# Kernel optimization log

Measured on AMD Instinct MI355X. Metric: run time of the kernel, lower is better.

Reference implementation:

```python
import jax, jax.numpy as jnp
import numpy as np

HEAD_NUM = 8
KEY_DIM = 16
EMBEDDING_DIM = 128
LOGIT_CLIPPING = 10.0

B, G, P, E = 512, 100, 100, 128


def setup_inputs() -> dict:
    key = jax.random.key(0)
    ks = jax.random.split(key, 9)
    return {
        "input1": jax.random.normal(ks[0], (B, 1, E), jnp.float32),
        "input2": jax.random.normal(ks[1], (B, G, E), jnp.float32),
        "remaining_loaded": jax.random.uniform(ks[2], (B, G, 1), jnp.float32),
        "ninf_mask": jnp.zeros((B, G, P), jnp.float32),
        "encoded_nodes": jax.random.normal(ks[3], (B, P, E), jnp.float32),
        "Wq": jax.random.normal(ks[4], (2 * E + 1, HEAD_NUM * KEY_DIM), jnp.float32) * 0.05,
        "Wk": jax.random.normal(ks[5], (E, HEAD_NUM * KEY_DIM), jnp.float32) * 0.05,
        "Wv": jax.random.normal(ks[6], (E, HEAD_NUM * KEY_DIM), jnp.float32) * 0.05,
        "Wc": jax.random.normal(ks[7], (HEAD_NUM * KEY_DIM, E), jnp.float32) * 0.05,
        "bc": jnp.zeros((E,), jnp.float32),
    }


def _heads(x):  # [B, N, H*K] -> [B, H, N, K]
    b, n, _ = x.shape
    return x.reshape(b, n, HEAD_NUM, KEY_DIM).transpose(0, 2, 1, 3)


def reference(input1, input2, remaining_loaded, ninf_mask, encoded_nodes, Wq, Wk, Wv, Wc, bc):
    group_s = input2.shape[1]
    # reset(): precompute keys/values from encoded nodes
    k = _heads(encoded_nodes @ Wk)  # [B,H,P,K]
    v = _heads(encoded_nodes @ Wv)  # [B,H,P,K]
    # forward()
    input_cat = jnp.concatenate(
        [jnp.broadcast_to(input1, (input1.shape[0], group_s, input1.shape[2])),
         input2, remaining_loaded], axis=2)  # [B,G,2E+1]
    q = _heads(input_cat @ Wq)  # [B,H,G,K]
    # multi-head attention with additive ninf mask
    score = jnp.einsum("bhgk,bhpk->bhgp", q, k) / np.sqrt(KEY_DIM).astype(np.float32)
    score = score + ninf_mask[:, None, :, :]
    weights = jax.nn.softmax(score, axis=3)
    out = jnp.einsum("bhgp,bhpk->bhgk", weights, v)  # [B,H,G,K]
    out_concat = out.transpose(0, 2, 1, 3).reshape(out.shape[0], group_s, HEAD_NUM * KEY_DIM)
    mh_atten_out = out_concat @ Wc + bc  # [B,G,E]
    # single-head pointer scoring with tanh clipping
    score2 = jnp.einsum("bge,bpe->bgp", mh_atten_out, encoded_nodes) / np.sqrt(EMBEDDING_DIM).astype(np.float32)
    score_masked = LOGIT_CLIPPING * jnp.tanh(score2) + ninf_mask
    probs = jax.nn.softmax(score_masked, axis=2)
    return probs
```

## Files before the change

kernel.cpp:

```cpp
#include <hip/hip_runtime.h>

#define NB 512
#define NG 100
#define NP 100
#define NE 128
#define NH 8

typedef __attribute__((ext_vector_type(8))) short short8;
typedef __attribute__((ext_vector_type(4))) short short4v;
typedef __attribute__((ext_vector_type(4))) float f32x4;

#define SE_STRIDE 128
#define SK_STRIDE 128
#define SVT_STRIDE 112
#define SE_BASE 0
#define SK_BASE (100 * 128)
#define SVT_BASE (SK_BASE + 100 * 128)
#define SMEM_SHORTS (SVT_BASE + 128 * 112)
#define SMEM_BYTES (SMEM_SHORTS * 2)

__device__ __forceinline__ short f2bf(float f) {
    union { float f; unsigned u; } v; v.f = f;
    unsigned r = v.u + 0x7FFFu + ((v.u >> 16) & 1u);
    return (short)(r >> 16);
}

__device__ __forceinline__ f32x4 mfma16(short4v a, short4v b, f32x4 c) {
#if __has_builtin(__builtin_amdgcn_mfma_f32_16x16x16_bf16)
    return __builtin_amdgcn_mfma_f32_16x16x16_bf16(a, b, c, 0, 0, 0);
#elif __has_builtin(__builtin_amdgcn_mfma_f32_16x16x16bf16_1k)
    return __builtin_amdgcn_mfma_f32_16x16x16bf16_1k(a, b, c, 0, 0, 0);
#else
    f32x4 d;
    asm volatile("v_mfma_f32_16x16x16_bf16 %0, %1, %2, %3"
                 : "=&v"(d) : "v"(a), "v"(b), "v"(c));
    return d;
#endif
}

__device__ __forceinline__ f32x4 mfma32(short8 a, short8 b, f32x4 c) {
    return __builtin_amdgcn_mfma_f32_16x16x32_bf16(a, b, c, 0, 0, 0);
}

__global__ void prep_kernel(const float* __restrict__ Wq, const float* __restrict__ Wk,
                            const float* __restrict__ Wv, const float* __restrict__ Wc,
                            short* __restrict__ WqT2, short* __restrict__ WkT,
                            short* __restrict__ WvT, short* __restrict__ WcT,
                            short* __restrict__ WqT1)
{
    int idx = blockIdx.x * 256 + threadIdx.x;
    int mat = idx >> 14;
    int e   = idx & 16383;
    int k = e >> 7, n = e & 127;
    float v;
    short* dst;
    if (mat == 0)      { v = Wq[(128 + k) * 128 + n]; dst = WqT2; }
    else if (mat == 1) { v = Wk[k * 128 + n];         dst = WkT;  }
    else if (mat == 2) { v = Wv[k * 128 + n];         dst = WvT;  }
    else if (mat == 3) { v = Wc[k * 128 + n];         dst = WcT;  }
    else               { v = Wq[k * 128 + n];         dst = WqT1; }
    dst[n * 128 + k] = f2bf(v);
}

__global__ __launch_bounds__(448, 2)
void fused_kernel(const float* __restrict__ input1, const float* __restrict__ input2,
                  const float* __restrict__ rem, const float* __restrict__ mask,
                  const float* __restrict__ enc, const float* __restrict__ Wq,
                  const float* __restrict__ bc,
                  const short* __restrict__ WqT2, const short* __restrict__ WkT,
                  const short* __restrict__ WvT, const short* __restrict__ WcT,
                  const short* __restrict__ WqT1, float* __restrict__ out)
{
    extern __shared__ short smem[];

    const int b    = blockIdx.x;
    const int tid  = threadIdx.x;
    const int wave = tid >> 6, lane = tid & 63;
    const int l16  = lane & 15, lh = lane >> 4;
    const int gt   = wave;
    const int g    = gt * 16 + l16;
    const bool gok = (g < NG);
    const float NINF = -__builtin_inff();

    {
        const f32x4* e4 = (const f32x4*)(enc + (size_t)b * NP * NE);
        for (int idx = tid; idx < NP * 32; idx += 448) {
            int row = idx >> 5, c = idx & 31;
            f32x4 v = e4[idx];
            short4v h = { f2bf(v[0]), f2bf(v[1]), f2bf(v[2]), f2bf(v[3]) };
            int off = (row * SE_STRIDE + c * 4) ^ ((row & 15) << 2);
            *(short4v*)(smem + SE_BASE + off) = h;
        }
        for (int idx = tid; idx < 128 * 3; idx += 448) {
            int row = idx / 3, c = 100 + (idx % 3) * 4;
            int off = (row * SVT_STRIDE + c) ^ ((row & 15) << 2);
            *(short4v*)(smem + SVT_BASE + off) = (short4v){0, 0, 0, 0};
        }
    }

    short4v qb[8];
    {
        const float* xrow = input2 + ((size_t)b * NG + g) * NE;
        const float* i1   = input1 + (size_t)b * NE;
        short8 xb[4], yb[4];
        #pragma unroll
        for (int ks = 0; ks < 4; ++ks) {
            f32x4 v0 = {0.f,0.f,0.f,0.f}, v1 = {0.f,0.f,0.f,0.f};
            if (gok) {
                v0 = *(const f32x4*)(xrow + ks * 32 + lh * 8);
                v1 = *(const f32x4*)(xrow + ks * 32 + lh * 8 + 4);
            }
            xb[ks] = (short8){ f2bf(v0[0]), f2bf(v0[1]), f2bf(v0[2]), f2bf(v0[3]),
                               f2bf(v1[0]), f2bf(v1[1]), f2bf(v1[2]), f2bf(v1[3]) };
            f32x4 u0 = *(const f32x4*)(i1 + ks * 32 + lh * 8);
            f32x4 u1 = *(const f32x4*)(i1 + ks * 32 + lh * 8 + 4);
            yb[ks] = (short8){ f2bf(u0[0]), f2bf(u0[1]), f2bf(u0[2]), f2bf(u0[3]),
                               f2bf(u1[0]), f2bf(u1[1]), f2bf(u1[2]), f2bf(u1[3]) };
        }
        float remv = gok ? rem[(size_t)b * NG + g] : 0.f;
        #pragma unroll
        for (int nt = 0; nt < 8; ++nt) {
            f32x4 acc0 = {0.f, 0.f, 0.f, 0.f}, acc1 = {0.f, 0.f, 0.f, 0.f};
            #pragma unroll
            for (int ks = 0; ks < 4; ++ks) {
                short8 a2 = *(const short8*)(WqT2 + (nt * 16 + l16) * NE + ks * 32 + lh * 8);
                acc0 = mfma32(a2, xb[ks], acc0);
                short8 a1 = *(const short8*)(WqT1 + (nt * 16 + l16) * NE + ks * 32 + lh * 8);
                acc1 = mfma32(a1, yb[ks], acc1);
            }
            f32x4 wlv = *(const f32x4*)(Wq + 256 * NE + nt * 16 + lh * 4);
            short4v q;
            #pragma unroll
            for (int r = 0; r < 4; ++r)
                q[r] = f2bf(0.25f * (acc0[r] + acc1[r] + remv * wlv[r]));
            qb[nt] = q;
        }
    }
    __syncthreads();

    for (int t = wave; t < 112; t += 7) {
        int mat = (t >= 56);
        int tt  = mat ? t - 56 : t;
        int mt = tt >> 3, nt = tt & 7;
        const short* WT = mat ? WvT : WkT;
        int arow = mt * 16 + l16;
        bool aok = (arow < NP);
        f32x4 acc0 = {0.f, 0.f, 0.f, 0.f}, acc1 = {0.f, 0.f, 0.f, 0.f};
        #pragma unroll
        for (int kt = 0; kt < 8; ++kt) {
            short4v a = {0, 0, 0, 0};
            if (aok) {
                int off = (arow * SE_STRIDE + kt * 16 + lh * 4) ^ ((arow & 15) << 2);
                a = *(const short4v*)(smem + SE_BASE + off);
            }
            short4v w = *(const short4v*)(WT + (nt * 16 + l16) * NE + kt * 16 + lh * 4);
            if (kt < 4) acc0 = mfma16(a, w, acc0);
            else        acc1 = mfma16(a, w, acc1);
        }
        f32x4 acc = acc0 + acc1;
        if (!mat) {
            #pragma unroll
            for (int r = 0; r < 4; ++r) {
                int p = mt * 16 + lh * 4 + r;
                if (p < NP) {
                    int off = (p * SK_STRIDE + nt * 16 + l16) ^ ((p & 15) << 2);
                    smem[SK_BASE + off] = f2bf(acc[r]);
                }
            }
        } else {
            int vrow = nt * 16 + l16;
            int p0 = mt * 16 + lh * 4;
            if (p0 < NP) {
                short4v h = { f2bf(acc[0]), f2bf(acc[1]), f2bf(acc[2]), f2bf(acc[3]) };
                int off = (vrow * SVT_STRIDE + p0) ^ ((vrow & 15) << 2);
                *(short4v*)(smem + SVT_BASE + off) = h;
            }
        }
    }

    float mk[7][4];
    {
        const float* mrow = mask + ((size_t)b * NG + g) * NP;
        #pragma unroll
        for (int pt = 0; pt < 7; ++pt)
            #pragma unroll
            for (int r = 0; r < 4; ++r) {
                int p = pt * 16 + lh * 4 + r;
                mk[pt][r] = (gok && p < NP) ? mrow[p] : NINF;
            }
    }
    __syncthreads();

    short4v ocb[8];
    #pragma unroll
    for (int h = 0; h < NH; ++h) {
        float vals[7][4];
        #pragma unroll
        for (int pt = 0; pt < 7; ++pt) {
            int prow = pt * 16 + l16;
            int off = (prow * SK_STRIDE + h * 16 + lh * 4) ^ ((prow & 15) << 2);
            short4v kf = *(const short4v*)(smem + SK_BASE + off);
            f32x4 z = {0.f, 0.f, 0.f, 0.f};
            f32x4 sc = mfma16(kf, qb[h], z);
            bool pv = (pt < 6) || (lh == 0);
            #pragma unroll
            for (int r = 0; r < 4; ++r)
                vals[pt][r] = pv ? sc[r] + mk[pt][r] : NINF;
        }
        float mr0 = vals[0][0], mr1 = vals[0][1], mr2 = vals[0][2], mr3 = vals[0][3];
        #pragma unroll
        for (int pt = 1; pt < 7; ++pt) {
            mr0 = fmaxf(mr0, vals[pt][0]); mr1 = fmaxf(mr1, vals[pt][1]);
            mr2 = fmaxf(mr2, vals[pt][2]); mr3 = fmaxf(mr3, vals[pt][3]);
        }
        float m = fmaxf(fmaxf(mr0, mr1), fmaxf(mr2, mr3));
        m = fmaxf(m, __shfl_xor(m, 16));
        m = fmaxf(m, __shfl_xor(m, 32));
        float s0 = 0.f, s1 = 0.f, s2 = 0.f, s3 = 0.f;
        #pragma unroll
        for (int pt = 0; pt < 7; ++pt) {
            float e0 = __expf(vals[pt][0] - m); vals[pt][0] = e0; s0 += e0;
            float e1 = __expf(vals[pt][1] - m); vals[pt][1] = e1; s1 += e1;
            float e2 = __expf(vals[pt][2] - m); vals[pt][2] = e2; s2 += e2;
            float e3 = __expf(vals[pt][3] - m); vals[pt][3] = e3; s3 += e3;
        }
        float s = (s0 + s1) + (s2 + s3);
        s += __shfl_xor(s, 16);
        s += __shfl_xor(s, 32);
        float inv = 1.f / s;
        f32x4 o0 = {0.f, 0.f, 0.f, 0.f}, o1 = {0.f, 0.f, 0.f, 0.f};
        #pragma unroll
        for (int pt = 0; pt < 7; ++pt) {
            short4v pb = { f2bf(vals[pt][0] * inv), f2bf(vals[pt][1] * inv),
                           f2bf(vals[pt][2] * inv), f2bf(vals[pt][3] * inv) };
            int vrow = h * 16 + l16;
            int off = (vrow * SVT_STRIDE + pt * 16 + lh * 4) ^ ((vrow & 15) << 2);
            short4v vf = *(const short4v*)(smem + SVT_BASE + off);
            if (pt & 1) o1 = mfma16(vf, pb, o1);
            else        o0 = mfma16(vf, pb, o0);
        }
        f32x4 o = o0 + o1;
        ocb[h] = (short4v){ f2bf(o[0]), f2bf(o[1]), f2bf(o[2]), f2bf(o[3]) };
    }

    short4v mhb[8];
    #pragma unroll
    for (int nt = 0; nt < 8; ++nt) {
        f32x4 acc0 = {0.f, 0.f, 0.f, 0.f}, acc1 = {0.f, 0.f, 0.f, 0.f};
        #pragma unroll
        for (int kt = 0; kt < 8; ++kt) {
            short4v a = *(const short4v*)(WcT + (nt * 16 + l16) * NE + kt * 16 + lh * 4);
            if (kt < 4) acc0 = mfma16(a, ocb[kt], acc0);
            else        acc1 = mfma16(a, ocb[kt], acc1);
        }
        f32x4 acc = acc0 + acc1;
        f32x4 bcv = *(const f32x4*)(bc + nt * 16 + lh * 4);
        mhb[nt] = (short4v){ f2bf((acc[0] + bcv[0]) * 0.08838834764831845f),
                             f2bf((acc[1] + bcv[1]) * 0.08838834764831845f),
                             f2bf((acc[2] + bcv[2]) * 0.08838834764831845f),
                             f2bf((acc[3] + bcv[3]) * 0.08838834764831845f) };
    }

    const float* mrow = mask + ((size_t)b * NG + g) * NP;
    float vals2[7][4];
    #pragma unroll
    for (int pt = 0; pt < 7; ++pt) {
        int prow = pt * 16 + l16;
        f32x4 acc0 = {0.f, 0.f, 0.f, 0.f}, acc1 = {0.f, 0.f, 0.f, 0.f};
        #pragma unroll
        for (int kt = 0; kt < 8; ++kt) {
            int off = (prow * SE_STRIDE + kt * 16 + lh * 4) ^ ((prow & 15) << 2);
            short4v ef = *(const short4v*)(smem + SE_BASE + off);
            if (kt < 4) acc0 = mfma16(ef, mhb[kt], acc0);
            else        acc1 = mfma16(ef, mhb[kt], acc1);
        }
        f32x4 acc = acc0 + acc1;
        #pragma unroll
        for (int r = 0; r < 4; ++r) {
            int p = pt * 16 + lh * 4 + r;
            bool pv = gok && (p < NP);
            float mkv = pv ? mrow[p] : NINF;
            float x = acc[r];
            float th = 1.f - 2.f / (__expf(2.f * x) + 1.f);
            vals2[pt][r] = pv ? 10.f * th + mkv : NINF;
        }
    }
    {
        float mr0 = vals2[0][0], mr1 = vals2[0][1], mr2 = vals2[0][2], mr3 = vals2[0][3];
        #pragma unroll
        for (int pt = 1; pt < 7; ++pt) {
            mr0 = fmaxf(mr0, vals2[pt][0]); mr1 = fmaxf(mr1, vals2[pt][1]);
            mr2 = fmaxf(mr2, vals2[pt][2]); mr3 = fmaxf(mr3, vals2[pt][3]);
        }
        float m = fmaxf(fmaxf(mr0, mr1), fmaxf(mr2, mr3));
        m = fmaxf(m, __shfl_xor(m, 16));
        m = fmaxf(m, __shfl_xor(m, 32));
        float s0 = 0.f, s1 = 0.f, s2 = 0.f, s3 = 0.f;
        #pragma unroll
        for (int pt = 0; pt < 7; ++pt) {
            float e0 = __expf(vals2[pt][0] - m); vals2[pt][0] = e0; s0 += e0;
            float e1 = __expf(vals2[pt][1] - m); vals2[pt][1] = e1; s1 += e1;
            float e2 = __expf(vals2[pt][2] - m); vals2[pt][2] = e2; s2 += e2;
            float e3 = __expf(vals2[pt][3] - m); vals2[pt][3] = e3; s3 += e3;
        }
        float s = (s0 + s1) + (s2 + s3);
        s += __shfl_xor(s, 16);
        s += __shfl_xor(s, 32);
        float inv = 1.f / s;
        float* orow = out + ((size_t)b * NG + g) * NP;
        #pragma unroll
        for (int pt = 0; pt < 7; ++pt)
            #pragma unroll
            for (int r = 0; r < 4; ++r) {
                int p = pt * 16 + lh * 4 + r;
                if (gok && p < NP) orow[p] = vals2[pt][r] * inv;
            }
    }
}

extern "C" void kernel_launch(void* const* d_in, const int* in_sizes, int n_in,
                              void* d_out, int out_size, void* d_ws, size_t ws_size,
                              hipStream_t stream)
{
    const float* input1 = (const float*)d_in[0];
    const float* input2 = (const float*)d_in[1];
    const float* rem    = (const float*)d_in[2];
    const float* mask   = (const float*)d_in[3];
    const float* enc    = (const float*)d_in[4];
    const float* Wq     = (const float*)d_in[5];
    const float* Wk     = (const float*)d_in[6];
    const float* Wv     = (const float*)d_in[7];
    const float* Wc     = (const float*)d_in[8];
    const float* bc     = (const float*)d_in[9];

    short* WqT2 = (short*)d_ws;
    short* WkT  = WqT2 + 16384;
    short* WvT  = WkT + 16384;
    short* WcT  = WvT + 16384;
    short* WqT1 = WcT + 16384;

    prep_kernel<<<320, 256, 0, stream>>>(Wq, Wk, Wv, Wc, WqT2, WkT, WvT, WcT, WqT1);

    hipFuncSetAttribute((const void*)fused_kernel,
                        hipFuncAttributeMaxDynamicSharedMemorySize, SMEM_BYTES);
    fused_kernel<<<NB, 448, SMEM_BYTES, stream>>>(
        input1, input2, rem, mask, enc, Wq, bc,
        WqT2, WkT, WvT, WcT, WqT1, (float*)d_out);
}
```

Baseline: 255.4 us.

## Drop shared encoded-node staging, compute K/V per wave into tiled shared layout

Stops staging the bf16 encoded nodes in shared memory. Each wave now loads its 16 encoded rows straight into registers and computes K and V with 16x16x32 MFMAs, writing them into 16x16 tile-blocked shared arrays with zero-padding. The pointer-scoring stage re-reads encoded nodes from global memory. Wc is pre-packed into 16x16 blocks, and mask loads and output stores are vectorized to float4. The aim is less LDS traffic and footprint, fewer swizzle computations and wider memory accesses, at the cost of extra global reads of enc in the last stage.

```diff
diff --git a/kernel.cpp b/kernel.cpp
--- a/kernel.cpp
+++ b/kernel.cpp
@@ -9,15 +9,6 @@
 typedef __attribute__((ext_vector_type(8))) short short8;
 typedef __attribute__((ext_vector_type(4))) short short4v;
 typedef __attribute__((ext_vector_type(4))) float f32x4;
-
-#define SE_STRIDE 128
-#define SK_STRIDE 128
-#define SVT_STRIDE 112
-#define SE_BASE 0
-#define SK_BASE (100 * 128)
-#define SVT_BASE (SK_BASE + 100 * 128)
-#define SMEM_SHORTS (SVT_BASE + 128 * 112)
-#define SMEM_BYTES (SMEM_SHORTS * 2)
 
 __device__ __forceinline__ short f2bf(float f) {
     union { float f; unsigned u; } v; v.f = f;
@@ -45,21 +36,19 @@
 __global__ void prep_kernel(const float* __restrict__ Wq, const float* __restrict__ Wk,
                             const float* __restrict__ Wv, const float* __restrict__ Wc,
                             short* __restrict__ WqT2, short* __restrict__ WkT,
-                            short* __restrict__ WvT, short* __restrict__ WcT,
-                            short* __restrict__ WqT1)
+                            short* __restrict__ WvT, short* __restrict__ WqT1,
+                            short* __restrict__ WcB)
 {
     int idx = blockIdx.x * 256 + threadIdx.x;
     int mat = idx >> 14;
     int e   = idx & 16383;
     int k = e >> 7, n = e & 127;
-    float v;
-    short* dst;
-    if (mat == 0)      { v = Wq[(128 + k) * 128 + n]; dst = WqT2; }
-    else if (mat == 1) { v = Wk[k * 128 + n];         dst = WkT;  }
-    else if (mat == 2) { v = Wv[k * 128 + n];         dst = WvT;  }
-    else if (mat == 3) { v = Wc[k * 128 + n];         dst = WcT;  }
-    else               { v = Wq[k * 128 + n];         dst = WqT1; }
-    dst[n * 128 + k] = f2bf(v);
+    if (mat == 0)      WqT2[n * 128 + k] = f2bf(Wq[(128 + k) * 128 + n]);
+    else if (mat == 1) WkT [n * 128 + k] = f2bf(Wk[k * 128 + n]);
+    else if (mat == 2) WvT [n * 128 + k] = f2bf(Wv[k * 128 + n]);
+    else if (mat == 3)
+        WcB[(((n >> 4) << 3) + (k >> 4)) * 256 + ((n & 15) << 4) + (k & 15)] = f2bf(Wc[k * 128 + n]);
+    else               WqT1[n * 128 + k] = f2bf(Wq[k * 128 + n]);
 }
 
 __global__ __launch_bounds__(448, 2)
@@ -68,35 +57,20 @@
                   const float* __restrict__ enc, const float* __restrict__ Wq,
                   const float* __restrict__ bc,
                   const short* __restrict__ WqT2, const short* __restrict__ WkT,
-                  const short* __restrict__ WvT, const short* __restrict__ WcT,
-                  const short* __restrict__ WqT1, float* __restrict__ out)
+                  const short* __restrict__ WvT, const short* __restrict__ WqT1,
+                  const short* __restrict__ WcB, float* __restrict__ out)
 {
-    extern __shared__ short smem[];
+    __shared__ short sKV[2 * 56 * 256];
+    short* sK = sKV;
+    short* sV = sKV + 56 * 256;
 
     const int b    = blockIdx.x;
     const int tid  = threadIdx.x;
     const int wave = tid >> 6, lane = tid & 63;
     const int l16  = lane & 15, lh = lane >> 4;
-    const int gt   = wave;
-    const int g    = gt * 16 + l16;
+    const int g    = wave * 16 + l16;
     const bool gok = (g < NG);
     const float NINF = -__builtin_inff();
-
-    {
-        const f32x4* e4 = (const f32x4*)(enc + (size_t)b * NP * NE);
-        for (int idx = tid; idx < NP * 32; idx += 448) {
-            int row = idx >> 5, c = idx & 31;
-            f32x4 v = e4[idx];
-            short4v h = { f2bf(v[0]), f2bf(v[1]), f2bf(v[2]), f2bf(v[3]) };
-            int off = (row * SE_STRIDE + c * 4) ^ ((row & 15) << 2);
-            *(short4v*)(smem + SE_BASE + off) = h;
-        }
-        for (int idx = tid; idx < 128 * 3; idx += 448) {
-            int row = idx / 3, c = 100 + (idx % 3) * 4;
-            int off = (row * SVT_STRIDE + c) ^ ((row & 15) << 2);
-            *(short4v*)(smem + SVT_BASE + off) = (short4v){0, 0, 0, 0};
-        }
-    }
 
     short4v qb[8];
     {
@@ -136,58 +110,61 @@
             qb[nt] = q;
         }
     }
-    __syncthreads();
-
-    for (int t = wave; t < 112; t += 7) {
-        int mat = (t >= 56);
-        int tt  = mat ? t - 56 : t;
-        int mt = tt >> 3, nt = tt & 7;
-        const short* WT = mat ? WvT : WkT;
-        int arow = mt * 16 + l16;
-        bool aok = (arow < NP);
-        f32x4 acc0 = {0.f, 0.f, 0.f, 0.f}, acc1 = {0.f, 0.f, 0.f, 0.f};
-        #pragma unroll
-        for (int kt = 0; kt < 8; ++kt) {
-            short4v a = {0, 0, 0, 0};
-            if (aok) {
-                int off = (arow * SE_STRIDE + kt * 16 + lh * 4) ^ ((arow & 15) << 2);
-                a = *(const short4v*)(smem + SE_BASE + off);
-            }
-            short4v w = *(const short4v*)(WT + (nt * 16 + l16) * NE + kt * 16 + lh * 4);
-            if (kt < 4) acc0 = mfma16(a, w, acc0);
-            else        acc1 = mfma16(a, w, acc1);
-        }
-        f32x4 acc = acc0 + acc1;
-        if (!mat) {
-            #pragma unroll
-            for (int r = 0; r < 4; ++r) {
-                int p = mt * 16 + lh * 4 + r;
-                if (p < NP) {
-                    int off = (p * SK_STRIDE + nt * 16 + l16) ^ ((p & 15) << 2);
-                    smem[SK_BASE + off] = f2bf(acc[r]);
-                }
-            }
-        } else {
-            int vrow = nt * 16 + l16;
-            int p0 = mt * 16 + lh * 4;
-            if (p0 < NP) {
-                short4v h = { f2bf(acc[0]), f2bf(acc[1]), f2bf(acc[2]), f2bf(acc[3]) };
-                int off = (vrow * SVT_STRIDE + p0) ^ ((vrow & 15) << 2);
-                *(short4v*)(smem + SVT_BASE + off) = h;
-            }
-        }
-    }
-
-    float mk[7][4];
+
     {
-        const float* mrow = mask + ((size_t)b * NG + g) * NP;
-        #pragma unroll
-        for (int pt = 0; pt < 7; ++pt)
-            #pragma unroll
-            for (int r = 0; r < 4; ++r) {
-                int p = pt * 16 + lh * 4 + r;
-                mk[pt][r] = (gok && p < NP) ? mrow[p] : NINF;
-            }
+        int row = wave * 16 + l16;
+        int rc  = row < NP ? row : NP - 1;
+        const float* er = enc + ((size_t)b * NP + rc) * NE;
+        short8 eb[4];
+        #pragma unroll
+        for (int ks = 0; ks < 4; ++ks) {
+            f32x4 u0 = *(const f32x4*)(er + ks * 32 + lh * 8);
+            f32x4 u1 = *(const f32x4*)(er + ks * 32 + lh * 8 + 4);
+            eb[ks] = (short8){ f2bf(u0[0]), f2bf(u0[1]), f2bf(u0[2]), f2bf(u0[3]),
+                               f2bf(u1[0]), f2bf(u1[1]), f2bf(u1[2]), f2bf(u1[3]) };
+        }
+        #pragma unroll
+        for (int h = 0; h < NH; ++h) {
+            f32x4 a0 = {0.f,0.f,0.f,0.f}, a1 = {0.f,0.f,0.f,0.f};
+            #pragma unroll
+            for (int ks = 0; ks < 4; ++ks) {
+                short8 w = *(const short8*)(WkT + (h * 16 + l16) * NE + ks * 32 + lh * 8);
+                if (ks < 2) a0 = mfma32(eb[ks], w, a0);
+                else        a1 = mfma32(eb[ks], w, a1);
+            }
+            f32x4 acc = a0 + a1;
+            int base = (h * 7 + wave) * 256;
+            #pragma unroll
+            for (int r = 0; r < 4; ++r)
+                sK[base + (lh * 4 + r) * 16 + l16] = f2bf(acc[r]);
+        }
+        #pragma unroll
+        for (int kb = 0; kb < 8; ++kb) {
+            f32x4 a0 = {0.f,0.f,0.f,0.f}, a1 = {0.f,0.f,0.f,0.f};
+            #pragma unroll
+            for (int ks = 0; ks < 4; ++ks) {
+                short8 a = *(const short8*)(WvT + (kb * 16 + l16) * NE + ks * 32 + lh * 8);
+                if (ks < 2) a0 = mfma32(a, eb[ks], a0);
+                else        a1 = mfma32(a, eb[ks], a1);
+            }
+            f32x4 acc = a0 + a1;
+            int base = (kb * 7 + wave) * 256;
+            bool pz = (wave == 6) && (l16 >= 4);
+            #pragma unroll
+            for (int r = 0; r < 4; ++r)
+                sV[base + (lh * 4 + r) * 16 + l16] = pz ? (short)0 : f2bf(acc[r]);
+        }
+    }
+
+    f32x4 mkv[7];
+    {
+        const float* mrow = mask + ((size_t)b * NG + (gok ? g : 0)) * NP;
+        #pragma unroll
+        for (int pt = 0; pt < 7; ++pt) {
+            bool ld = gok && (pt < 6 || lh == 0);
+            mkv[pt] = ld ? *(const f32x4*)(mrow + pt * 16 + lh * 4)
+                         : (f32x4){NINF, NINF, NINF, NINF};
+        }
     }
     __syncthreads();
 
@@ -197,15 +174,12 @@
         float vals[7][4];
         #pragma unroll
         for (int pt = 0; pt < 7; ++pt) {
-            int prow = pt * 16 + l16;
-            int off = (prow * SK_STRIDE + h * 16 + lh * 4) ^ ((prow & 15) << 2);
-            short4v kf = *(const short4v*)(smem + SK_BASE + off);
+            short4v kf = *(const short4v*)(sK + (h * 7 + pt) * 256 + l16 * 16 + lh * 4);
             f32x4 z = {0.f, 0.f, 0.f, 0.f};
             f32x4 sc = mfma16(kf, qb[h], z);
-            bool pv = (pt < 6) || (lh == 0);
             #pragma unroll
             for (int r = 0; r < 4; ++r)
-                vals[pt][r] = pv ? sc[r] + mk[pt][r] : NINF;
+                vals[pt][r] = sc[r] + mkv[pt][r];
         }
         float mr0 = vals[0][0], mr1 = vals[0][1], mr2 = vals[0][2], mr3 = vals[0][3];
         #pragma unroll
@@ -233,9 +207,7 @@
         for (int pt = 0; pt < 7; ++pt) {
             short4v pb = { f2bf(vals[pt][0] * inv), f2bf(vals[pt][1] * inv),
                            f2bf(vals[pt][2] * inv), f2bf(vals[pt][3] * inv) };
-            int vrow = h * 16 + l16;
-            int off = (vrow * SVT_STRIDE + pt * 16 + lh * 4) ^ ((vrow & 15) << 2);
-            short4v vf = *(const short4v*)(smem + SVT_BASE + off);
+            short4v vf = *(const short4v*)(sV + (h * 7 + pt) * 256 + l16 * 16 + lh * 4);
             if (pt & 1) o1 = mfma16(vf, pb, o1);
             else        o0 = mfma16(vf, pb, o0);
         }
@@ -249,7 +221,7 @@
         f32x4 acc0 = {0.f, 0.f, 0.f, 0.f}, acc1 = {0.f, 0.f, 0.f, 0.f};
         #pragma unroll
         for (int kt = 0; kt < 8; ++kt) {
-            short4v a = *(const short4v*)(WcT + (nt * 16 + l16) * NE + kt * 16 + lh * 4);
+            short4v a = *(const short4v*)(WcB + (nt * 8 + kt) * 256 + l16 * 16 + lh * 4);
             if (kt < 4) acc0 = mfma16(a, ocb[kt], acc0);
             else        acc1 = mfma16(a, ocb[kt], acc1);
         }
@@ -261,28 +233,30 @@
                              f2bf((acc[3] + bcv[3]) * 0.08838834764831845f) };
     }
 
-    const float* mrow = mask + ((size_t)b * NG + g) * NP;
+    const float* encb = enc + (size_t)b * NP * NE;
+    const float* mrow = mask + ((size_t)b * NG + (gok ? g : 0)) * NP;
     float vals2[7][4];
     #pragma unroll
     for (int pt = 0; pt < 7; ++pt) {
         int prow = pt * 16 + l16;
-        f32x4 acc0 = {0.f, 0.f, 0.f, 0.f}, acc1 = {0.f, 0.f, 0.f, 0.f};
+        const float* erow = encb + (size_t)(prow < NP ? prow : NP - 1) * NE;
+        f32x4 a0 = {0.f,0.f,0.f,0.f}, a1 = {0.f,0.f,0.f,0.f};
         #pragma unroll
         for (int kt = 0; kt < 8; ++kt) {
-            int off = (prow * SE_STRIDE + kt * 16 + lh * 4) ^ ((prow & 15) << 2);
-            short4v ef = *(const short4v*)(smem + SE_BASE + off);
-            if (kt < 4) acc0 = mfma16(ef, mhb[kt], acc0);
-            else        acc1 = mfma16(ef, mhb[kt], acc1);
-        }
-        f32x4 acc = acc0 + acc1;
+            f32x4 ev = *(const f32x4*)(erow + kt * 16 + lh * 4);
+            short4v ef = { f2bf(ev[0]), f2bf(ev[1]), f2bf(ev[2]), f2bf(ev[3]) };
+            if (kt < 4) a0 = mfma16(ef, mhb[kt], a0);
+            else        a1 = mfma16(ef, mhb[kt], a1);
+        }
+        f32x4 acc = a0 + a1;
+        bool ld = gok && (pt < 6 || lh == 0);
+        f32x4 mv = ld ? *(const f32x4*)(mrow + pt * 16 + lh * 4)
+                      : (f32x4){NINF, NINF, NINF, NINF};
         #pragma unroll
         for (int r = 0; r < 4; ++r) {
-            int p = pt * 16 + lh * 4 + r;
-            bool pv = gok && (p < NP);
-            float mkv = pv ? mrow[p] : NINF;
             float x = acc[r];
             float th = 1.f - 2.f / (__expf(2.f * x) + 1.f);
-            vals2[pt][r] = pv ? 10.f * th + mkv : NINF;
+            vals2[pt][r] = 10.f * th + mv[r];
         }
     }
     {
@@ -309,12 +283,14 @@
         float inv = 1.f / s;
         float* orow = out + ((size_t)b * NG + g) * NP;
         #pragma unroll
-        for (int pt = 0; pt < 7; ++pt)
-            #pragma unroll
-            for (int r = 0; r < 4; ++r) {
-                int p = pt * 16 + lh * 4 + r;
-                if (gok && p < NP) orow[p] = vals2[pt][r] * inv;
-            }
+        for (int pt = 0; pt < 7; ++pt) {
+            bool st = gok && (pt < 6 || lh == 0);
+            if (st) {
+                f32x4 ov = { vals2[pt][0] * inv, vals2[pt][1] * inv,
+                             vals2[pt][2] * inv, vals2[pt][3] * inv };
+                *(f32x4*)(orow + pt * 16 + lh * 4) = ov;
+            }
+        }
     }
 }
 
@@ -336,14 +312,12 @@
     short* WqT2 = (short*)d_ws;
     short* WkT  = WqT2 + 16384;
     short* WvT  = WkT + 16384;
-    short* WcT  = WvT + 16384;
-    short* WqT1 = WcT + 16384;
-
-    prep_kernel<<<320, 256, 0, stream>>>(Wq, Wk, Wv, Wc, WqT2, WkT, WvT, WcT, WqT1);
-
-    hipFuncSetAttribute((const void*)fused_kernel,
-                        hipFuncAttributeMaxDynamicSharedMemorySize, SMEM_BYTES);
-    fused_kernel<<<NB, 448, SMEM_BYTES, stream>>>(
+    short* WqT1 = WvT + 16384;
+    short* WcB  = WqT1 + 16384;
+
+    prep_kernel<<<320, 256, 0, stream>>>(Wq, Wk, Wv, Wc, WqT2, WkT, WvT, WqT1, WcB);
+
+    fused_kernel<<<NB, 448, 0, stream>>>(
         input1, input2, rem, mask, enc, Wq, bc,
-        WqT2, WkT, WvT, WcT, WqT1, (float*)d_out);
-}
+        WqT2, WkT, WvT, WqT1, WcB, (float*)d_out);
+}
```

New measurement: 217.2 us. -15.0%, faster.
